# Kernel optimization log

Measured on AMD Instinct MI355X. Metric: run time of the kernel, lower is better.

## Reference

```python
import jax, jax.numpy as jnp
import numpy as np

# FP4 e2m1 lookup: nibble -> value (bit3 = sign, bits2:0 = e2m1 magnitude)
FP4_LUT = jnp.array([0.0, 0.5, 1.0, 1.5, 2.0, 3.0, 4.0, 6.0,
                     -0.0, -0.5, -1.0, -1.5, -2.0, -3.0, -4.0, -6.0], dtype=jnp.float32)
BLOCK = 16  # elements per micro-scale (one uint8 E8M0 scale per 16 fp4 values)


def _dequant(packed, sf):
    """packed: [R, K//2] int bytes (two fp4 nibbles each, low nibble first).
    sf: [R, K//16] E8M0 exponents (value = 2^(sf-127)). Returns [R, K] f32."""
    R, Kh = packed.shape
    K = Kh * 2
    lo = packed & 0xF
    hi = (packed >> 4) & 0xF
    nib = jnp.stack([lo, hi], axis=-1).reshape(R, K)
    vals = FP4_LUT[nib]  # [R, K]
    block_scale = jnp.exp2((sf - 127).astype(jnp.float32))  # [R, K//16]
    return (vals.reshape(R, K // BLOCK, BLOCK) * block_scale[:, :, None]).reshape(R, K)


def setup_inputs() -> dict:
    key = jax.random.key(0)
    ks = jax.random.split(key, 6)
    M, N, K = 8192, 4096, 4224  # K = in_features(4096) + select_num(128)
    A_packed = jax.random.randint(ks[0], (M, K // 2), 0, 256, dtype=jnp.int32)
    SFA = jax.random.randint(ks[1], (M, K // BLOCK), 118, 134, dtype=jnp.int32)
    B_packed = jax.random.randint(ks[2], (N, K // 2), 0, 256, dtype=jnp.int32)
    SFB = jax.random.randint(ks[3], (N, K // BLOCK), 118, 134, dtype=jnp.int32)
    scale = jax.random.uniform(ks[4], (1,), dtype=jnp.float32, minval=0.5, maxval=1.5)
    bias = jax.random.normal(ks[5], (N,), dtype=jnp.float32)
    return {"A_packed": A_packed, "SFA": SFA, "scale": scale,
            "B_packed": B_packed, "SFB": SFB, "bias": bias}


def reference(A_packed, SFA, scale, B_packed, SFB, bias):
    A = _dequant(A_packed, SFA)        # [M, K]
    B = _dequant(B_packed, SFB)        # [N, K]
    # y = scale * (A @ B^T) + bias   (self.scale == 1.0 folded into scale)
    y = scale[0] * jnp.einsum('mk,nk->mn', A, B) + bias[None, :]
    return y
```

## Files before the change

### kernel.cpp

```cpp
#include <hip/hip_runtime.h>
#include <stdint.h>

#define M_DIM 8192
#define N_DIM 4096
#define K_DIM 4224
#define BK 64

typedef float f32x16 __attribute__((ext_vector_type(16)));
typedef int   i32x8  __attribute__((ext_vector_type(8)));
typedef int   i32x4  __attribute__((ext_vector_type(4)));

#define RAW_BARRIER()  asm volatile("s_barrier" ::: "memory")
#define WAIT_VM8()     asm volatile("s_waitcnt vmcnt(8)" ::: "memory")
#define WAIT_VM0()     asm volatile("s_waitcnt vmcnt(0)" ::: "memory")

__device__ __forceinline__ uint32_t conv4(uint32_t x, uint32_t k1) {
    uint32_t n7   = x & 0x07070707u;
    uint32_t base = __builtin_amdgcn_perm(0x46444240u, 0x3E3C3800u, n7);
    uint32_t nz   = __builtin_amdgcn_perm(0x01010101u, 0x01010100u, n7);
    uint32_t sign = (x & 0x08080808u) << 4;
    return (base + nz * k1 - (nz << 6)) | sign;
}

__global__ __launch_bounds__(256) void dequant_all(
    const int* __restrict__ Ap, const int* __restrict__ SFA, uint8_t* __restrict__ Aout,
    const int* __restrict__ Bp, const int* __restrict__ SFB, uint8_t* __restrict__ Bout)
{
    const int nhA = M_DIM * K_DIM / 32;
    int i = blockIdx.x * 256 + threadIdx.x;
    const int* p; const int* sf; uint8_t* out; int idx;
    if (i < nhA) { p = Ap; sf = SFA; out = Aout; idx = i; }
    else         { p = Bp; sf = SFB; out = Bout; idx = i - nhA; }

    const int4* p4 = (const int4*)p;
    int4 q0 = p4[4 * idx];
    int4 q1 = p4[4 * idx + 1];
    int4 q2 = p4[4 * idx + 2];
    int4 q3 = p4[4 * idx + 3];
    int2 sfp = ((const int2*)sf)[idx];
    uint32_t k1a = (uint32_t)(((sfp.x - 127) << 2) + 64);
    uint32_t k1b = (uint32_t)(((sfp.y - 127) << 2) + 64);

    uint32_t o[8];
#pragma unroll
    for (int g = 0; g < 4; ++g) {
        int4 pg = (g == 0) ? q0 : (g == 1) ? q1 : (g == 2) ? q2 : q3;
        uint32_t k1 = (g < 2) ? k1a : k1b;
        uint32_t w = (uint32_t)(pg.x & 0xFF) | ((uint32_t)(pg.y & 0xFF) << 8) |
                     ((uint32_t)(pg.z & 0xFF) << 16) | ((uint32_t)pg.w << 24);
        uint32_t lr = conv4(w & 0x0F0F0F0Fu, k1);
        uint32_t hr = conv4((w >> 4) & 0x0F0F0F0Fu, k1);
        o[2 * g]     = __builtin_amdgcn_perm(hr, lr, 0x05010400u);
        o[2 * g + 1] = __builtin_amdgcn_perm(hr, lr, 0x07030602u);
    }
    *(uint4*)(out + (size_t)idx * 32)      = make_uint4(o[0], o[1], o[2], o[3]);
    *(uint4*)(out + (size_t)idx * 32 + 16) = make_uint4(o[4], o[5], o[6], o[7]);
}

__global__ __launch_bounds__(256, 1) void gemm_mx(
    const uint8_t* __restrict__ A, const uint8_t* __restrict__ B,
    const float* __restrict__ scale, const float* __restrict__ bias,
    float* __restrict__ C)
{
    __shared__ uint8_t smem[131072];

    const int tid  = threadIdx.x;
    const int lane = tid & 63;
    const int w    = tid >> 6;
    const int wm   = w >> 1;
    const int wn   = w & 1;
    const int r31  = lane & 31;
    const int h    = lane >> 5;

    const int lin = blockIdx.y * 16 + blockIdx.x;
    const int o   = (lin & 7) * 64 + (lin >> 3);
    const int bn0 = (o & 15) * 256;
    const int bm0 = (o >> 4) * 256;

    f32x16 acc[4][4];
#pragma unroll
    for (int i = 0; i < 4; ++i)
#pragma unroll
        for (int j = 0; j < 4; ++j)
            acc[i][j] = (f32x16)(0.0f);

    const int srow = lane >> 2;
    const int scol = (((lane & 3) ^ ((lane >> 3) & 3)) << 4);
    const uint8_t* Ag = A + (size_t)(bm0 + w * 64 + srow) * K_DIM + scol;
    const uint8_t* Bg = B + (size_t)(bn0 + w * 64 + srow) * K_DIM + scol;
    uint8_t* Asw = smem + w * 4096;
    uint8_t* Bsw = smem + 16384 + w * 4096;

#define GLDS(gp, lp)                                                             \
    __builtin_amdgcn_global_load_lds(                                            \
        (const __attribute__((address_space(1))) void*)(gp),                     \
        (__attribute__((address_space(3))) void*)(lp), 16, 0, 0)

#define STAGE(koff, boff)                                                        \
    do {                                                                         \
        const uint8_t* ag_ = Ag + (koff);                                        \
        const uint8_t* bg_ = Bg + (koff);                                        \
        GLDS(ag_,                       Asw + (boff));                           \
        GLDS(ag_ + (size_t)16 * K_DIM,  Asw + (boff) + 1024);                    \
        GLDS(ag_ + (size_t)32 * K_DIM,  Asw + (boff) + 2048);                    \
        GLDS(ag_ + (size_t)48 * K_DIM,  Asw + (boff) + 3072);                    \
        GLDS(bg_,                       Bsw + (boff));                           \
        GLDS(bg_ + (size_t)16 * K_DIM,  Bsw + (boff) + 1024);                    \
        GLDS(bg_ + (size_t)32 * K_DIM,  Bsw + (boff) + 2048);                    \
        GLDS(bg_ + (size_t)48 * K_DIM,  Bsw + (boff) + 3072);                    \
    } while (0)

    const int sx = (r31 >> 1) & 3;
    const uint8_t* pa_lo[4]; const uint8_t* pa_hi[4];
    const uint8_t* pb_lo[4]; const uint8_t* pb_hi[4];
#pragma unroll
    for (int mi = 0; mi < 4; ++mi) {
        const uint8_t* base = smem + (wm * 128 + mi * 32 + r31) * 64;
        pa_lo[mi] = base + (((2 * h)     ^ sx) << 4);
        pa_hi[mi] = base + (((2 * h + 1) ^ sx) << 4);
    }
#pragma unroll
    for (int ni = 0; ni < 4; ++ni) {
        const uint8_t* base = smem + 16384 + (wn * 128 + ni * 32 + r31) * 64;
        pb_lo[ni] = base + (((2 * h)     ^ sx) << 4);
        pb_hi[ni] = base + (((2 * h + 1) ^ sx) << 4);
    }

    i32x8 afX0[4], afX1[4], bfX0[4], bfX1[4];

    auto rd = [&](const uint8_t* plo, const uint8_t* phi, int off, i32x8& dst) {
        i32x4 lo = *(const i32x4*)(plo + off);
        i32x4 hi = *(const i32x4*)(phi + off);
        dst = __builtin_shufflevector(lo, hi, 0, 1, 2, 3, 4, 5, 6, 7);
    };
    auto mm = [&](const i32x8& a, const i32x8& b, f32x16& c) {
        c = __builtin_amdgcn_mfma_scale_f32_32x32x64_f8f6f4(
                a, b, c, 1, 1, 0, 0x7F7F7F7F, 0, 0x7F7F7F7F);
    };

#define CLUSTER(AC, BC, MI)                                   \
    __builtin_amdgcn_s_setprio(1);                            \
    mm(AC[MI], BC[0], acc[MI][0]); mm(AC[MI], BC[1], acc[MI][1]); \
    mm(AC[MI], BC[2], acc[MI][2]); mm(AC[MI], BC[3], acc[MI][3]); \
    __builtin_amdgcn_s_setprio(0);

#define CORE(AC, BC, AN, BN, OBN)                             \
    CLUSTER(AC, BC, 0)                                        \
    rd(pa_lo[0], pa_hi[0], OBN, AN[0]);                       \
    rd(pb_lo[0], pb_hi[0], OBN, BN[0]);                       \
    CLUSTER(AC, BC, 1)                                        \
    rd(pa_lo[1], pa_hi[1], OBN, AN[1]);                       \
    rd(pb_lo[1], pb_hi[1], OBN, BN[1]);                       \
    CLUSTER(AC, BC, 2)                                        \
    rd(pa_lo[2], pa_hi[2], OBN, AN[2]);                       \
    rd(pb_lo[2], pb_hi[2], OBN, BN[2]);                       \
    CLUSTER(AC, BC, 3)                                        \
    rd(pa_lo[3], pa_hi[3], OBN, AN[3]);                       \
    rd(pb_lo[3], pb_hi[3], OBN, BN[3]);

#define BODY(T, AC, BC, AN, BN, OBN, OBS)                     \
    STAGE(((T) + 3) * BK, OBS);                               \
    CORE(AC, BC, AN, BN, OBN)                                 \
    WAIT_VM8(); RAW_BARRIER();

    STAGE(0 * BK, 0);
    STAGE(1 * BK, 32768);
    STAGE(2 * BK, 65536);
    WAIT_VM8();
    RAW_BARRIER();
    rd(pa_lo[0], pa_hi[0], 0, afX0[0]);
    rd(pa_lo[1], pa_hi[1], 0, afX0[1]);
    rd(pa_lo[2], pa_hi[2], 0, afX0[2]);
    rd(pa_lo[3], pa_hi[3], 0, afX0[3]);
    rd(pb_lo[0], pb_hi[0], 0, bfX0[0]);
    rd(pb_lo[1], pb_hi[1], 0, bfX0[1]);
    rd(pb_lo[2], pb_hi[2], 0, bfX0[2]);
    rd(pb_lo[3], pb_hi[3], 0, bfX0[3]);

#pragma unroll 1
    for (int g = 0; g < 15; ++g) {
        BODY(4 * g,     afX0, bfX0, afX1, bfX1, 32768, 98304)
        BODY(4 * g + 1, afX1, bfX1, afX0, bfX0, 65536, 0)
        BODY(4 * g + 2, afX0, bfX0, afX1, bfX1, 98304, 32768)
        BODY(4 * g + 3, afX1, bfX1, afX0, bfX0, 0,     65536)
    }
    BODY(60, afX0, bfX0, afX1, bfX1, 32768, 98304)
    BODY(61, afX1, bfX1, afX0, bfX0, 65536, 0)
    BODY(62, afX0, bfX0, afX1, bfX1, 98304, 32768)
    CORE(afX1, bfX1, afX0, bfX0, 0)
    WAIT_VM0(); RAW_BARRIER();
    CORE(afX0, bfX0, afX1, bfX1, 32768)
    CLUSTER(afX1, bfX1, 0)
    CLUSTER(afX1, bfX1, 1)
    CLUSTER(afX1, bfX1, 2)
    CLUSTER(afX1, bfX1, 3)
#undef BODY
#undef CORE
#undef CLUSTER
#undef STAGE
#undef GLDS

    const float sc = scale[0];
#pragma unroll
    for (int ni = 0; ni < 4; ++ni) {
        const int col = bn0 + wn * 128 + ni * 32 + r31;
        const float bv = bias[col];
#pragma unroll
        for (int mi = 0; mi < 4; ++mi) {
            const int rbase = bm0 + wm * 128 + mi * 32 + 4 * h;
#pragma unroll
            for (int reg = 0; reg < 16; ++reg) {
                const int row = rbase + (reg & 3) + 8 * (reg >> 2);
                C[(size_t)row * N_DIM + col] = sc * acc[mi][ni][reg] + bv;
            }
        }
    }
}

extern "C" void kernel_launch(void* const* d_in, const int* in_sizes, int n_in,
                              void* d_out, int out_size, void* d_ws, size_t ws_size,
                              hipStream_t stream) {
    const int*   A_packed = (const int*)d_in[0];
    const int*   SFA      = (const int*)d_in[1];
    const float* scale    = (const float*)d_in[2];
    const int*   B_packed = (const int*)d_in[3];
    const int*   SFB      = (const int*)d_in[4];
    const float* bias     = (const float*)d_in[5];
    float*       out      = (float*)d_out;

    uint8_t* Abf8 = (uint8_t*)d_ws;
    uint8_t* Bbf8 = Abf8 + (size_t)M_DIM * K_DIM;

    const int npairA = M_DIM * K_DIM / 32;
    const int npairB = N_DIM * K_DIM / 32;
    dequant_all<<<(npairA + npairB) / 256, 256, 0, stream>>>(
        A_packed, SFA, Abf8, B_packed, SFB, Bbf8);

    dim3 grid(N_DIM / 256, M_DIM / 256);
    gemm_mx<<<grid, 256, 0, stream>>>(Abf8, Bbf8, scale, bias, out);
}
```

Before: 336.8 us.

## Enlarge GEMM block tile to 512x256 with 8 waves and triple-buffered LDS

Each workgroup now has 512 threads (8 waves) and computes a 512x256 output tile, so every loaded B tile is reused across twice as many rows of A and total B traffic per output drops. The LDS pipeline becomes a three-stage ring of 48 KB buffers with prefetch distance 2, and each thread issues six global-to-LDS loads per stage. Register fragments are no longer double-buffered: fragments are read from LDS just before their MFMA clusters, which removes the overlap between LDS reads and matrix math. The launch bound now asks for 512 threads with a minimum of 2 blocks, which may force a low per-wave register cap while the 256-float accumulator per thread is unchanged, so spilling is a risk.

```diff
diff --git a/kernel.cpp b/kernel.cpp
--- a/kernel.cpp
+++ b/kernel.cpp
@@ -11,7 +11,7 @@
 typedef int   i32x4  __attribute__((ext_vector_type(4)));
 
 #define RAW_BARRIER()  asm volatile("s_barrier" ::: "memory")
-#define WAIT_VM8()     asm volatile("s_waitcnt vmcnt(8)" ::: "memory")
+#define WAIT_VM6()     asm volatile("s_waitcnt vmcnt(6)" ::: "memory")
 #define WAIT_VM0()     asm volatile("s_waitcnt vmcnt(0)" ::: "memory")
 
 __device__ __forceinline__ uint32_t conv4(uint32_t x, uint32_t k1) {
@@ -57,12 +57,12 @@
     *(uint4*)(out + (size_t)idx * 32 + 16) = make_uint4(o[4], o[5], o[6], o[7]);
 }
 
-__global__ __launch_bounds__(256, 1) void gemm_mx(
+__global__ __launch_bounds__(512, 2) void gemm_mx(
     const uint8_t* __restrict__ A, const uint8_t* __restrict__ B,
     const float* __restrict__ scale, const float* __restrict__ bias,
     float* __restrict__ C)
 {
-    __shared__ uint8_t smem[131072];
+    __shared__ uint8_t smem[147456];
 
     const int tid  = threadIdx.x;
     const int lane = tid & 63;
@@ -73,9 +73,9 @@
     const int h    = lane >> 5;
 
     const int lin = blockIdx.y * 16 + blockIdx.x;
-    const int o   = (lin & 7) * 64 + (lin >> 3);
+    const int o   = (lin & 7) * 32 + (lin >> 3);
     const int bn0 = (o & 15) * 256;
-    const int bm0 = (o >> 4) * 256;
+    const int bm0 = (o >> 4) * 512;
 
     f32x16 acc[4][4];
 #pragma unroll
@@ -87,9 +87,9 @@
     const int srow = lane >> 2;
     const int scol = (((lane & 3) ^ ((lane >> 3) & 3)) << 4);
     const uint8_t* Ag = A + (size_t)(bm0 + w * 64 + srow) * K_DIM + scol;
-    const uint8_t* Bg = B + (size_t)(bn0 + w * 64 + srow) * K_DIM + scol;
+    const uint8_t* Bg = B + (size_t)(bn0 + w * 32 + srow) * K_DIM + scol;
     uint8_t* Asw = smem + w * 4096;
-    uint8_t* Bsw = smem + 16384 + w * 4096;
+    uint8_t* Bsw = smem + 32768 + w * 2048;
 
 #define GLDS(gp, lp)                                                             \
     __builtin_amdgcn_global_load_lds(                                            \
@@ -106,8 +106,6 @@
         GLDS(ag_ + (size_t)48 * K_DIM,  Asw + (boff) + 3072);                    \
         GLDS(bg_,                       Bsw + (boff));                           \
         GLDS(bg_ + (size_t)16 * K_DIM,  Bsw + (boff) + 1024);                    \
-        GLDS(bg_ + (size_t)32 * K_DIM,  Bsw + (boff) + 2048);                    \
-        GLDS(bg_ + (size_t)48 * K_DIM,  Bsw + (boff) + 3072);                    \
     } while (0)
 
     const int sx = (r31 >> 1) & 3;
@@ -121,12 +119,12 @@
     }
 #pragma unroll
     for (int ni = 0; ni < 4; ++ni) {
-        const uint8_t* base = smem + 16384 + (wn * 128 + ni * 32 + r31) * 64;
+        const uint8_t* base = smem + 32768 + (wn * 128 + ni * 32 + r31) * 64;
         pb_lo[ni] = base + (((2 * h)     ^ sx) << 4);
         pb_hi[ni] = base + (((2 * h + 1) ^ sx) << 4);
     }
 
-    i32x8 afX0[4], afX1[4], bfX0[4], bfX1[4];
+    i32x8 af[4], bf[4];
 
     auto rd = [&](const uint8_t* plo, const uint8_t* phi, int off, i32x8& dst) {
         i32x4 lo = *(const i32x4*)(plo + off);
@@ -138,62 +136,47 @@
                 a, b, c, 1, 1, 0, 0x7F7F7F7F, 0, 0x7F7F7F7F);
     };
 
-#define CLUSTER(AC, BC, MI)                                   \
+#define CLUSTER(MI)                                           \
     __builtin_amdgcn_s_setprio(1);                            \
-    mm(AC[MI], BC[0], acc[MI][0]); mm(AC[MI], BC[1], acc[MI][1]); \
-    mm(AC[MI], BC[2], acc[MI][2]); mm(AC[MI], BC[3], acc[MI][3]); \
+    mm(af[MI], bf[0], acc[MI][0]); mm(af[MI], bf[1], acc[MI][1]); \
+    mm(af[MI], bf[2], acc[MI][2]); mm(af[MI], bf[3], acc[MI][3]); \
     __builtin_amdgcn_s_setprio(0);
 
-#define CORE(AC, BC, AN, BN, OBN)                             \
-    CLUSTER(AC, BC, 0)                                        \
-    rd(pa_lo[0], pa_hi[0], OBN, AN[0]);                       \
-    rd(pb_lo[0], pb_hi[0], OBN, BN[0]);                       \
-    CLUSTER(AC, BC, 1)                                        \
-    rd(pa_lo[1], pa_hi[1], OBN, AN[1]);                       \
-    rd(pb_lo[1], pb_hi[1], OBN, BN[1]);                       \
-    CLUSTER(AC, BC, 2)                                        \
-    rd(pa_lo[2], pa_hi[2], OBN, AN[2]);                       \
-    rd(pb_lo[2], pb_hi[2], OBN, BN[2]);                       \
-    CLUSTER(AC, BC, 3)                                        \
-    rd(pa_lo[3], pa_hi[3], OBN, AN[3]);                       \
-    rd(pb_lo[3], pb_hi[3], OBN, BN[3]);
-
-#define BODY(T, AC, BC, AN, BN, OBN, OBS)                     \
-    STAGE(((T) + 3) * BK, OBS);                               \
-    CORE(AC, BC, AN, BN, OBN)                                 \
-    WAIT_VM8(); RAW_BARRIER();
+#define CORE(OB)                                              \
+    rd(pa_lo[0], pa_hi[0], OB, af[0]);                        \
+    rd(pb_lo[0], pb_hi[0], OB, bf[0]);                        \
+    rd(pb_lo[1], pb_hi[1], OB, bf[1]);                        \
+    rd(pb_lo[2], pb_hi[2], OB, bf[2]);                        \
+    rd(pb_lo[3], pb_hi[3], OB, bf[3]);                        \
+    CLUSTER(0)                                                \
+    rd(pa_lo[1], pa_hi[1], OB, af[1]);                        \
+    CLUSTER(1)                                                \
+    rd(pa_lo[2], pa_hi[2], OB, af[2]);                        \
+    CLUSTER(2)                                                \
+    rd(pa_lo[3], pa_hi[3], OB, af[3]);                        \
+    CLUSTER(3)
+
+#define BODY(T, OBCUR, OBS)                                   \
+    STAGE(((T) + 2) * BK, OBS);                               \
+    CORE(OBCUR)                                               \
+    WAIT_VM6(); RAW_BARRIER();
 
     STAGE(0 * BK, 0);
-    STAGE(1 * BK, 32768);
-    STAGE(2 * BK, 65536);
-    WAIT_VM8();
+    STAGE(1 * BK, 49152);
+    WAIT_VM6();
     RAW_BARRIER();
-    rd(pa_lo[0], pa_hi[0], 0, afX0[0]);
-    rd(pa_lo[1], pa_hi[1], 0, afX0[1]);
-    rd(pa_lo[2], pa_hi[2], 0, afX0[2]);
-    rd(pa_lo[3], pa_hi[3], 0, afX0[3]);
-    rd(pb_lo[0], pb_hi[0], 0, bfX0[0]);
-    rd(pb_lo[1], pb_hi[1], 0, bfX0[1]);
-    rd(pb_lo[2], pb_hi[2], 0, bfX0[2]);
-    rd(pb_lo[3], pb_hi[3], 0, bfX0[3]);
 
 #pragma unroll 1
-    for (int g = 0; g < 15; ++g) {
-        BODY(4 * g,     afX0, bfX0, afX1, bfX1, 32768, 98304)
-        BODY(4 * g + 1, afX1, bfX1, afX0, bfX0, 65536, 0)
-        BODY(4 * g + 2, afX0, bfX0, afX1, bfX1, 98304, 32768)
-        BODY(4 * g + 3, afX1, bfX1, afX0, bfX0, 0,     65536)
-    }
-    BODY(60, afX0, bfX0, afX1, bfX1, 32768, 98304)
-    BODY(61, afX1, bfX1, afX0, bfX0, 65536, 0)
-    BODY(62, afX0, bfX0, afX1, bfX1, 98304, 32768)
-    CORE(afX1, bfX1, afX0, bfX0, 0)
+    for (int g = 0; g < 21; ++g) {
+        const int t = 3 * g;
+        BODY(t,     0,     98304)
+        BODY(t + 1, 49152, 0)
+        BODY(t + 2, 98304, 49152)
+    }
+    BODY(63, 0, 98304)
+    CORE(49152)
     WAIT_VM0(); RAW_BARRIER();
-    CORE(afX0, bfX0, afX1, bfX1, 32768)
-    CLUSTER(afX1, bfX1, 0)
-    CLUSTER(afX1, bfX1, 1)
-    CLUSTER(afX1, bfX1, 2)
-    CLUSTER(afX1, bfX1, 3)
+    CORE(98304)
 #undef BODY
 #undef CORE
 #undef CLUSTER
@@ -236,6 +219,6 @@
     dequant_all<<<(npairA + npairB) / 256, 256, 0, stream>>>(
         A_packed, SFA, Abf8, B_packed, SFB, Bbf8);
 
-    dim3 grid(N_DIM / 256, M_DIM / 256);
-    gemm_mx<<<grid, 256, 0, stream>>>(Abf8, Bbf8, scale, bias, out);
-}
+    dim3 grid(N_DIM / 256, M_DIM / 512);
+    gemm_mx<<<grid, 512, 0, stream>>>(Abf8, Bbf8, scale, bias, out);
+}
```

Measured after the change: 1.164 ms. +245.6%, slower.
